# Optimization experiments

Measured on AMD Instinct MI355X. Metric: run time of the kernel, lower is better.

## Reference

```python
import jax, jax.numpy as jnp
import numpy as np


def _seg_mean(feat_src, src, dst, n_tgt):
    # gather neighbor features along edges, scatter-mean onto targets
    g = feat_src[src]                                   # [E, D]
    s = jax.ops.segment_sum(g, dst, num_segments=n_tgt)  # [n_tgt, D]
    cnt = jax.ops.segment_sum(jnp.ones((src.shape[0],), feat_src.dtype), dst,
                              num_segments=n_tgt)
    return s / jnp.clip(cnt, 1.0)[:, None]


def setup_inputs() -> dict:
    key = jax.random.key(0)
    ks = jax.random.split(key, 12)
    N0, N1, N2 = 1000000, 400000, 100000
    E0, E1 = 2000000, 500000
    D, H, O = 128, 50, 1
    return {
        "x": jax.random.normal(ks[0], (N0, D), jnp.float32),
        "edge_attr": jnp.ones((N0,), jnp.float32),  # unused by forward, kept for signature parity
        "src0": jax.random.randint(ks[1], (E0,), 0, N0),
        "dst0": jax.random.randint(ks[2], (E0,), 0, N1),
        "src1": jax.random.randint(ks[3], (E1,), 0, N1),
        "dst1": jax.random.randint(ks[4], (E1,), 0, N2),
        "n1": N1,
        "n2": N2,
        "Wl1": jax.random.normal(ks[5], (D, H), jnp.float32) / np.sqrt(D),
        "bl1": jnp.zeros((H,), jnp.float32),
        "Wr1": jax.random.normal(ks[6], (D, H), jnp.float32) / np.sqrt(D),
        "Wl2": jax.random.normal(ks[7], (H, H), jnp.float32) / np.sqrt(H),
        "bl2": jnp.zeros((H,), jnp.float32),
        "Wr2": jax.random.normal(ks[8], (H, H), jnp.float32) / np.sqrt(H),
        "Wo": jax.random.normal(ks[9], (H, O), jnp.float32) / np.sqrt(H),
        "bo": jnp.zeros((O,), jnp.float32),
    }


def reference(x, edge_attr, src0, dst0, src1, dst1, n1, n2,
              Wl1, bl1, Wr1, Wl2, bl2, Wr2, Wo, bo):
    # Layer 1: SAGEConv((x, x[:n1]), edge_index0)  -> [n1, H]
    agg1 = _seg_mean(x, src0, dst0, n1)
    h = agg1 @ Wl1 + bl1 + x[:n1] @ Wr1
    h = jax.nn.relu(h)  # inter-layer ReLU (dropout p=0.0 is a no-op)
    # Layer 2: SAGEConv((h, h[:n2]), edge_index1)  -> [n2, H]
    agg2 = _seg_mean(h, src1, dst1, n2)
    h2 = agg2 @ Wl2 + bl2 + h[:n2] @ Wr2
    # Final Linear + ReLU
    return jax.nn.relu(h2 @ Wo + bo)
```

## Files before the change

### kernel.cpp

```cpp
#include <hip/hip_runtime.h>

#define N0V 1000000
#define N1V 400000
#define N2V 100000
#define E0V 2000000
#define E1V 500000
#define DD  128
#define HH  50
#define FP  64
#define KC  32
#define NB_SCAN 1563

#define OFF_DEG    0ULL
#define OFF_SSUM   1600000ULL
#define OFF_CNT2   2000000ULL
#define ZERO_BYTES 2400000ULL
#define OFF_ROWPTR 2400000ULL
#define OFF_CURSOR 4000000ULL
#define OFF_BSUM   5600000ULL
#define OFF_SMALL  5608192ULL
#define OFF_WL1P   5609216ULL
#define OFF_WR1P   5641984ULL
#define OFF_S      5674752ULL
#define OFF_T      7274752ULL
#define OFF_CSR    7674752ULL
#define OFF_AGG    15674752ULL
#define OFF_Y      118074752ULL
#define WS_NEEDED  246074752ULL

__device__ inline unsigned short f2bf(float f) {
    unsigned int u = __float_as_uint(f);
    unsigned int r = (u + 0x7FFFu + ((u >> 16) & 1u)) >> 16;
    return (unsigned short)r;
}

__global__ void pad_w(const float* __restrict__ Wl1, const float* __restrict__ Wr1,
                      const float* __restrict__ bl1,
                      const float* __restrict__ Wl2, const float* __restrict__ bl2,
                      const float* __restrict__ Wr2, const float* __restrict__ Wo,
                      const float* __restrict__ bo,
                      float* __restrict__ Wl1p, float* __restrict__ Wr1p,
                      float* __restrict__ smalls)
{
    int gid = blockIdx.x * 256 + threadIdx.x;
    if (gid < 128 * FP) {
        int k = gid >> 6, f = gid & 63;
        float a = (f < HH) ? Wl1[k * HH + f] : 0.f;
        float b = (f < HH) ? Wr1[k * HH + f] : 0.f;
        Wl1p[gid] = a;
        Wr1p[gid] = b;
    }
    if (gid < FP) {
        float a = 0.f, b = 0.f;
        if (gid < HH) {
            for (int g = 0; g < HH; ++g) {
                float w = Wo[g];
                a += Wl2[gid * HH + g] * w;
                b += Wr2[gid * HH + g] * w;
            }
        }
        smalls[gid]          = (gid < HH) ? bl1[gid] : 0.f;
        smalls[FP + gid]     = a;
        smalls[2 * FP + gid] = b;
    }
    if (gid == 0) {
        float c = bo[0];
        for (int g = 0; g < HH; ++g) c += bl2[g] * Wo[g];
        smalls[3 * FP] = c;
    }
}

__global__ __launch_bounds__(256, 4) void gemm_y(const float* __restrict__ X,
                                                 const float* __restrict__ Wp,
                                                 unsigned int* __restrict__ Ybf)
{
    __shared__ float xs[KC * 256];
    const int t  = threadIdx.x;
    const int n0 = blockIdx.x * 256;
    const int ng = t >> 3;
    const int fg = t & 7;
    const int nbase = n0 + ng * 8;

    float acc[8][8];
#pragma unroll
    for (int i = 0; i < 8; ++i)
#pragma unroll
        for (int j = 0; j < 8; ++j) acc[i][j] = 0.f;

    for (int c = 0; c < DD / KC; ++c) {
        if (c) __syncthreads();
#pragma unroll
        for (int j = 0; j < 8; ++j) {
            int f4  = j * 256 + t;
            int row = f4 >> 3;
            int c4  = f4 & 7;
            int gn  = n0 + row;
            float4 v = make_float4(0.f, 0.f, 0.f, 0.f);
            if (gn < N0V) v = *(const float4*)(X + (size_t)gn * DD + c * KC + c4 * 4);
            int kb  = c4 * 4;
            int rsw = row ^ (c4 << 3);
            xs[(kb + 0) * 256 + rsw] = v.x;
            xs[(kb + 1) * 256 + rsw] = v.y;
            xs[(kb + 2) * 256 + rsw] = v.z;
            xs[(kb + 3) * 256 + rsw] = v.w;
        }
        __syncthreads();
#pragma unroll 4
        for (int kk = 0; kk < KC; ++kk) {
            int m = kk >> 2;
            const float* xp = &xs[kk * 256 + ((ng ^ m) << 3)];
            float4 x0 = *(const float4*)xp;
            float4 x1 = *(const float4*)(xp + 4);
            const float* wr = Wp + (size_t)(c * KC + kk) * FP + fg * 8;
            float4 w0 = *(const float4*)wr;
            float4 w1 = *(const float4*)(wr + 4);
            float xv[8] = {x0.x, x0.y, x0.z, x0.w, x1.x, x1.y, x1.z, x1.w};
            float wv[8] = {w0.x, w0.y, w0.z, w0.w, w1.x, w1.y, w1.z, w1.w};
#pragma unroll
            for (int i = 0; i < 8; ++i)
#pragma unroll
                for (int j = 0; j < 8; ++j)
                    acc[i][j] = fmaf(xv[i], wv[j], acc[i][j]);
        }
    }

    if (nbase < N0V) {
#pragma unroll
        for (int i = 0; i < 8; ++i) {
            uint4 q;
            q.x = (unsigned)f2bf(acc[i][0]) | ((unsigned)f2bf(acc[i][1]) << 16);
            q.y = (unsigned)f2bf(acc[i][2]) | ((unsigned)f2bf(acc[i][3]) << 16);
            q.z = (unsigned)f2bf(acc[i][4]) | ((unsigned)f2bf(acc[i][5]) << 16);
            q.w = (unsigned)f2bf(acc[i][6]) | ((unsigned)f2bf(acc[i][7]) << 16);
            *(uint4*)(Ybf + (size_t)(nbase + i) * 32 + fg * 4) = q;
        }
    }
}

__global__ __launch_bounds__(256) void hist1(const int* __restrict__ dst,
                                             int* __restrict__ deg)
{
    int e = blockIdx.x * 256 + threadIdx.x;
    if (e < E0V) atomicAdd(&deg[dst[e]], 1);
}

__global__ __launch_bounds__(256) void scan_a(const int* __restrict__ deg,
                                              int* __restrict__ incl,
                                              int* __restrict__ bsum)
{
    __shared__ int s[256];
    int tid = threadIdx.x;
    int i = blockIdx.x * 256 + tid;
    int v = (i < N1V) ? deg[i] : 0;
    s[tid] = v;
    __syncthreads();
#pragma unroll
    for (int off = 1; off < 256; off <<= 1) {
        int tv = (tid >= off) ? s[tid - off] : 0;
        __syncthreads();
        s[tid] += tv;
        __syncthreads();
    }
    if (i < N1V) incl[i] = s[tid];
    if (tid == 255) bsum[blockIdx.x] = s[255];
}

__global__ __launch_bounds__(256) void scan_b(int* __restrict__ bsum)
{
    __shared__ int s[256];
    __shared__ int run_s;
    int tid = threadIdx.x;
    if (tid == 0) run_s = 0;
    __syncthreads();
    for (int base = 0; base < NB_SCAN; base += 256) {
        int idx = base + tid;
        int v = (idx < NB_SCAN) ? bsum[idx] : 0;
        s[tid] = v;
        __syncthreads();
#pragma unroll
        for (int off = 1; off < 256; off <<= 1) {
            int tv = (tid >= off) ? s[tid - off] : 0;
            __syncthreads();
            s[tid] += tv;
            __syncthreads();
        }
        int rbase = run_s;
        if (idx < NB_SCAN) bsum[idx] = s[tid] - v + rbase;
        __syncthreads();
        if (tid == 255) run_s = rbase + s[255];
        __syncthreads();
    }
}

__global__ __launch_bounds__(256) void scan_c(const int* __restrict__ deg,
                                              int* __restrict__ rowptr,
                                              int* __restrict__ cursor,
                                              const int* __restrict__ bsum)
{
    int i = blockIdx.x * 256 + threadIdx.x;
    if (i < N1V) {
        int ex = rowptr[i] - deg[i] + bsum[blockIdx.x];
        rowptr[i] = ex;
        cursor[i] = ex;
    }
}

__global__ __launch_bounds__(256) void fill1(const int* __restrict__ src,
                                             const int* __restrict__ dst,
                                             int* __restrict__ cursor,
                                             int* __restrict__ csr)
{
    int e = blockIdx.x * 256 + threadIdx.x;
    if (e < E0V) {
        int d = dst[e];
        int pos = atomicAdd(&cursor[d], 1);
        csr[pos] = src[e];
    }
}

__global__ __launch_bounds__(256) void gather1(const unsigned int* __restrict__ Ybf,
                                               const int* __restrict__ rowptr,
                                               const int* __restrict__ deg,
                                               const int* __restrict__ csr,
                                               float* __restrict__ agg)
{
    int node = blockIdx.x * 8 + (threadIdx.x >> 5);
    int lane = threadIdx.x & 31;
    if (node >= N1V) return;
    int start = rowptr[node];
    int dg = deg[node];
    float a0 = 0.f, a1 = 0.f, b0 = 0.f, b1 = 0.f;
    int k = 0;
    for (; k + 1 < dg; k += 2) {
        int s0 = csr[start + k];
        int s1 = csr[start + k + 1];
        unsigned v0 = Ybf[(size_t)s0 * 32 + lane];
        unsigned v1 = Ybf[(size_t)s1 * 32 + lane];
        a0 += __uint_as_float(v0 << 16);
        a1 += __uint_as_float(v0 & 0xFFFF0000u);
        b0 += __uint_as_float(v1 << 16);
        b1 += __uint_as_float(v1 & 0xFFFF0000u);
    }
    if (k < dg) {
        int s0 = csr[start + k];
        unsigned v0 = Ybf[(size_t)s0 * 32 + lane];
        a0 += __uint_as_float(v0 << 16);
        a1 += __uint_as_float(v0 & 0xFFFF0000u);
    }
    a0 += b0;
    a1 += b1;
    float inv = 1.0f / (float)max(dg, 1);
    *(float2*)(agg + (size_t)node * FP + lane * 2) = make_float2(a0 * inv, a1 * inv);
}

__global__ __launch_bounds__(256, 4) void node_l1(const float* __restrict__ X,
                                                  const float* __restrict__ Wp,
                                                  const float* __restrict__ agg,
                                                  const float* __restrict__ smalls,
                                                  float* __restrict__ sArr,
                                                  float* __restrict__ tArr)
{
    __shared__ float xs[KC * 256];
    const int t  = threadIdx.x;
    const int n0 = blockIdx.x * 256;
    const int ng = t >> 3;
    const int fg = t & 7;
    const int nbase = n0 + ng * 8;

    float acc[8][8];
#pragma unroll
    for (int i = 0; i < 8; ++i)
#pragma unroll
        for (int j = 0; j < 8; ++j) acc[i][j] = 0.f;

    for (int c = 0; c < DD / KC; ++c) {
        if (c) __syncthreads();
#pragma unroll
        for (int j = 0; j < 8; ++j) {
            int f4  = j * 256 + t;
            int row = f4 >> 3;
            int c4  = f4 & 7;
            int gn  = n0 + row;
            float4 v = make_float4(0.f, 0.f, 0.f, 0.f);
            if (gn < N1V) v = *(const float4*)(X + (size_t)gn * DD + c * KC + c4 * 4);
            int kb  = c4 * 4;
            int rsw = row ^ (c4 << 3);
            xs[(kb + 0) * 256 + rsw] = v.x;
            xs[(kb + 1) * 256 + rsw] = v.y;
            xs[(kb + 2) * 256 + rsw] = v.z;
            xs[(kb + 3) * 256 + rsw] = v.w;
        }
        __syncthreads();
#pragma unroll 4
        for (int kk = 0; kk < KC; ++kk) {
            int m = kk >> 2;
            const float* xp = &xs[kk * 256 + ((ng ^ m) << 3)];
            float4 x0 = *(const float4*)xp;
            float4 x1 = *(const float4*)(xp + 4);
            const float* wr = Wp + (size_t)(c * KC + kk) * FP + fg * 8;
            float4 w0 = *(const float4*)wr;
            float4 w1 = *(const float4*)(wr + 4);
            float xv[8] = {x0.x, x0.y, x0.z, x0.w, x1.x, x1.y, x1.z, x1.w};
            float wv[8] = {w0.x, w0.y, w0.z, w0.w, w1.x, w1.y, w1.z, w1.w};
#pragma unroll
            for (int i = 0; i < 8; ++i)
#pragma unroll
                for (int j = 0; j < 8; ++j)
                    acc[i][j] = fmaf(xv[i], wv[j], acc[i][j]);
        }
    }

    if (nbase >= N1V) return;

    const float* blp = smalls + fg * 8;
    const float* wAp = smalls + FP + fg * 8;
    const float* wBp = smalls + 2 * FP + fg * 8;
    float bl_r[8], wA_r[8], wB_r[8];
#pragma unroll
    for (int j = 0; j < 8; ++j) { bl_r[j] = blp[j]; wA_r[j] = wAp[j]; wB_r[j] = wBp[j]; }

    float ps[8], pt[8];
#pragma unroll
    for (int i = 0; i < 8; ++i) {
        int n = nbase + i;
        const float* ar = agg + (size_t)n * FP + fg * 8;
        float4 a0 = *(const float4*)ar;
        float4 a1 = *(const float4*)(ar + 4);
        float agf[8] = {a0.x, a0.y, a0.z, a0.w, a1.x, a1.y, a1.z, a1.w};
        float s_acc = 0.f, t_acc = 0.f;
#pragma unroll
        for (int j = 0; j < 8; ++j) {
            float h = fmaxf(agf[j] + bl_r[j] + acc[i][j], 0.f);
            s_acc = fmaf(h, wA_r[j], s_acc);
            t_acc = fmaf(h, wB_r[j], t_acc);
        }
        ps[i] = s_acc; pt[i] = t_acc;
    }
#pragma unroll
    for (int i = 0; i < 8; ++i) {
#pragma unroll
        for (int m = 1; m < 8; m <<= 1) {
            ps[i] += __shfl_xor(ps[i], m);
            pt[i] += __shfl_xor(pt[i], m);
        }
    }
    if (fg == 0) {
#pragma unroll
        for (int i = 0; i < 8; ++i) sArr[nbase + i] = ps[i];
        if (nbase < N2V) {
#pragma unroll
            for (int i = 0; i < 8; ++i) tArr[nbase + i] = pt[i];
        }
    }
}

__global__ __launch_bounds__(256) void scatter2(const float* __restrict__ sArr,
                                                const int* __restrict__ src,
                                                const int* __restrict__ dst,
                                                float* __restrict__ ssum,
                                                float* __restrict__ cnt2)
{
    int e = blockIdx.x * 256 + threadIdx.x;
    if (e >= E1V) return;
    int sI = src[e];
    int dI = dst[e];
    atomicAdd(&ssum[dI], sArr[sI]);
    atomicAdd(&cnt2[dI], 1.0f);
}

__global__ __launch_bounds__(256) void final_out(const float* __restrict__ ssum,
                                                 const float* __restrict__ cnt2,
                                                 const float* __restrict__ tArr,
                                                 const float* __restrict__ smalls,
                                                 float* __restrict__ out)
{
    int i = blockIdx.x * 256 + threadIdx.x;
    if (i >= N2V) return;
    float c = smalls[3 * FP];
    float inv = 1.0f / fmaxf(cnt2[i], 1.0f);
    float o = fmaf(ssum[i], inv, tArr[i] + c);
    out[i] = fmaxf(o, 0.f);
}

extern "C" void kernel_launch(void* const* d_in, const int* in_sizes, int n_in,
                              void* d_out, int out_size, void* d_ws, size_t ws_size,
                              hipStream_t stream)
{
    if (ws_size < WS_NEEDED) return;

    const float* x    = (const float*)d_in[0];
    const int*   src0 = (const int*)d_in[2];
    const int*   dst0 = (const int*)d_in[3];
    const int*   src1 = (const int*)d_in[4];
    const int*   dst1 = (const int*)d_in[5];
    const float* Wl1  = (const float*)d_in[8];
    const float* bl1  = (const float*)d_in[9];
    const float* Wr1  = (const float*)d_in[10];
    const float* Wl2  = (const float*)d_in[11];
    const float* bl2  = (const float*)d_in[12];
    const float* Wr2  = (const float*)d_in[13];
    const float* Wo   = (const float*)d_in[14];
    const float* bo   = (const float*)d_in[15];
    float* out = (float*)d_out;

    char* ws = (char*)d_ws;
    int*   deg    = (int*)(ws + OFF_DEG);
    float* ssum   = (float*)(ws + OFF_SSUM);
    float* cnt2   = (float*)(ws + OFF_CNT2);
    int*   rowptr = (int*)(ws + OFF_ROWPTR);
    int*   cursor = (int*)(ws + OFF_CURSOR);
    int*   bsum   = (int*)(ws + OFF_BSUM);
    float* smalls = (float*)(ws + OFF_SMALL);
    float* Wl1p   = (float*)(ws + OFF_WL1P);
    float* Wr1p   = (float*)(ws + OFF_WR1P);
    float* sArr   = (float*)(ws + OFF_S);
    float* tArr   = (float*)(ws + OFF_T);
    int*   csr    = (int*)(ws + OFF_CSR);
    float* agg    = (float*)(ws + OFF_AGG);
    unsigned int* ybf = (unsigned int*)(ws + OFF_Y);

    hipMemsetAsync(d_ws, 0, ZERO_BYTES, stream);

    pad_w<<<32, 256, 0, stream>>>(Wl1, Wr1, bl1, Wl2, bl2, Wr2, Wo, bo, Wl1p, Wr1p, smalls);

    gemm_y<<<(N0V + 255) / 256, 256, 0, stream>>>(x, Wl1p, ybf);

    hist1<<<(E0V + 255) / 256, 256, 0, stream>>>(dst0, deg);
    scan_a<<<NB_SCAN, 256, 0, stream>>>(deg, rowptr, bsum);
    scan_b<<<1, 256, 0, stream>>>(bsum);
    scan_c<<<NB_SCAN, 256, 0, stream>>>(deg, rowptr, cursor, bsum);
    fill1<<<(E0V + 255) / 256, 256, 0, stream>>>(src0, dst0, cursor, csr);

    gather1<<<(N1V + 7) / 8, 256, 0, stream>>>(ybf, rowptr, deg, csr, agg);

    node_l1<<<NB_SCAN, 256, 0, stream>>>(x, Wr1p, agg, smalls, sArr, tArr);

    scatter2<<<(E1V + 255) / 256, 256, 0, stream>>>(sArr, src1, dst1, ssum, cnt2);

    final_out<<<(N2V + 255) / 256, 256, 0, stream>>>(ssum, cnt2, tArr, smalls, out);
}
```

Baseline: 1.490 ms.

## Fuse both layer-1 GEMMs into one MFMA fp16 kernel with fp16 intermediates

Replaces the two scalar FP32 GEMM kernels (x@Wl1 for all nodes and x[:n1]@Wr1) with one kernel that converts x tiles to fp16 in shared memory and uses 16x16x32 f16 MFMA instructions. It computes both products in a single pass over x, removing the second read of x[:n1]. Y, the root term D and the aggregated features are now stored as packed fp16 rather than bf16/fp32, and a lightweight epilogue kernel replaces node_l1. This targets the FLOP-bound scalar GEMM and redundant x reads, at the cost of reduced precision and a larger D buffer.

New measurement: 1.237 ms. 1.21x faster.

```diff
diff --git a/kernel.cpp b/kernel.cpp
--- a/kernel.cpp
+++ b/kernel.cpp
@@ -8,7 +8,6 @@
 #define DD  128
 #define HH  50
 #define FP  64
-#define KC  32
 #define NB_SCAN 1563
 
 #define OFF_DEG    0ULL
@@ -19,19 +18,30 @@
 #define OFF_CURSOR 4000000ULL
 #define OFF_BSUM   5600000ULL
 #define OFF_SMALL  5608192ULL
-#define OFF_WL1P   5609216ULL
-#define OFF_WR1P   5641984ULL
-#define OFF_S      5674752ULL
-#define OFF_T      7274752ULL
-#define OFF_CSR    7674752ULL
-#define OFF_AGG    15674752ULL
-#define OFF_Y      118074752ULL
-#define WS_NEEDED  246074752ULL
-
-__device__ inline unsigned short f2bf(float f) {
-    unsigned int u = __float_as_uint(f);
-    unsigned int r = (u + 0x7FFFu + ((u >> 16) & 1u)) >> 16;
-    return (unsigned short)r;
+#define OFF_WLT    5609216ULL
+#define OFF_WRT    5625600ULL
+#define OFF_S      5641984ULL
+#define OFF_T      7241984ULL
+#define OFF_CSR    7641984ULL
+#define OFF_AGG    15641984ULL
+#define OFF_D      66841984ULL
+#define OFF_Y      118041984ULL
+#define WS_NEEDED  246041984ULL
+
+typedef _Float16 half8 __attribute__((ext_vector_type(8)));
+typedef _Float16 half4 __attribute__((ext_vector_type(4)));
+typedef float    f32x4 __attribute__((ext_vector_type(4)));
+
+__device__ inline unsigned pack2h(float a, float b) {
+    union { _Float16 h[2]; unsigned u; } cv;
+    cv.h[0] = (_Float16)a;
+    cv.h[1] = (_Float16)b;
+    return cv.u;
+}
+__device__ inline float2 unp2h(unsigned v) {
+    union { unsigned u; _Float16 h[2]; } cv;
+    cv.u = v;
+    return make_float2((float)cv.h[0], (float)cv.h[1]);
 }
 
 __global__ void pad_w(const float* __restrict__ Wl1, const float* __restrict__ Wr1,
@@ -39,16 +49,16 @@
                       const float* __restrict__ Wl2, const float* __restrict__ bl2,
                       const float* __restrict__ Wr2, const float* __restrict__ Wo,
                       const float* __restrict__ bo,
-                      float* __restrict__ Wl1p, float* __restrict__ Wr1p,
+                      _Float16* __restrict__ Wlt, _Float16* __restrict__ Wrt,
                       float* __restrict__ smalls)
 {
     int gid = blockIdx.x * 256 + threadIdx.x;
-    if (gid < 128 * FP) {
-        int k = gid >> 6, f = gid & 63;
-        float a = (f < HH) ? Wl1[k * HH + f] : 0.f;
-        float b = (f < HH) ? Wr1[k * HH + f] : 0.f;
-        Wl1p[gid] = a;
-        Wr1p[gid] = b;
+    if (gid < 64 * 128) {
+        int n = gid >> 7, k = gid & 127;
+        float a = (n < HH) ? Wl1[k * HH + n] : 0.f;
+        float b = (n < HH) ? Wr1[k * HH + n] : 0.f;
+        Wlt[gid] = (_Float16)a;
+        Wrt[gid] = (_Float16)b;
     }
     if (gid < FP) {
         float a = 0.f, b = 0.f;
@@ -70,69 +80,97 @@
     }
 }
 
-__global__ __launch_bounds__(256, 4) void gemm_y(const float* __restrict__ X,
-                                                 const float* __restrict__ Wp,
-                                                 unsigned int* __restrict__ Ybf)
-{
-    __shared__ float xs[KC * 256];
+__global__ __launch_bounds__(256, 3) void fused_gemm(
+    const float* __restrict__ X,
+    const _Float16* __restrict__ Wlt,
+    const _Float16* __restrict__ Wrt,
+    unsigned int* __restrict__ Yh,
+    unsigned int* __restrict__ Dh)
+{
+    __shared__ _Float16 xs[128][72];
     const int t  = threadIdx.x;
-    const int n0 = blockIdx.x * 256;
-    const int ng = t >> 3;
-    const int fg = t & 7;
-    const int nbase = n0 + ng * 8;
-
-    float acc[8][8];
-#pragma unroll
-    for (int i = 0; i < 8; ++i)
-#pragma unroll
-        for (int j = 0; j < 8; ++j) acc[i][j] = 0.f;
-
-    for (int c = 0; c < DD / KC; ++c) {
+    const int w  = t >> 6;
+    const int l  = t & 63;
+    const int lr = l & 15;
+    const int lk = l >> 4;
+    const int n0 = blockIdx.x * 128;
+    const bool hasD = (blockIdx.x < N1V / 128);
+
+    f32x4 yacc[4][2], dacc[4][2];
+#pragma unroll
+    for (int ft = 0; ft < 4; ++ft)
+#pragma unroll
+        for (int mt = 0; mt < 2; ++mt) {
+            yacc[ft][mt] = (f32x4){0.f, 0.f, 0.f, 0.f};
+            dacc[ft][mt] = (f32x4){0.f, 0.f, 0.f, 0.f};
+        }
+
+    const int srow = t >> 4;
+    const int scol = t & 15;
+
+    for (int c = 0; c < 2; ++c) {
         if (c) __syncthreads();
 #pragma unroll
-        for (int j = 0; j < 8; ++j) {
-            int f4  = j * 256 + t;
-            int row = f4 >> 3;
-            int c4  = f4 & 7;
+        for (int p = 0; p < 8; ++p) {
+            int row = p * 16 + srow;
             int gn  = n0 + row;
             float4 v = make_float4(0.f, 0.f, 0.f, 0.f);
-            if (gn < N0V) v = *(const float4*)(X + (size_t)gn * DD + c * KC + c4 * 4);
-            int kb  = c4 * 4;
-            int rsw = row ^ (c4 << 3);
-            xs[(kb + 0) * 256 + rsw] = v.x;
-            xs[(kb + 1) * 256 + rsw] = v.y;
-            xs[(kb + 2) * 256 + rsw] = v.z;
-            xs[(kb + 3) * 256 + rsw] = v.w;
-        }
-        __syncthreads();
-#pragma unroll 4
-        for (int kk = 0; kk < KC; ++kk) {
-            int m = kk >> 2;
-            const float* xp = &xs[kk * 256 + ((ng ^ m) << 3)];
-            float4 x0 = *(const float4*)xp;
-            float4 x1 = *(const float4*)(xp + 4);
-            const float* wr = Wp + (size_t)(c * KC + kk) * FP + fg * 8;
-            float4 w0 = *(const float4*)wr;
-            float4 w1 = *(const float4*)(wr + 4);
-            float xv[8] = {x0.x, x0.y, x0.z, x0.w, x1.x, x1.y, x1.z, x1.w};
-            float wv[8] = {w0.x, w0.y, w0.z, w0.w, w1.x, w1.y, w1.z, w1.w};
-#pragma unroll
-            for (int i = 0; i < 8; ++i)
-#pragma unroll
-                for (int j = 0; j < 8; ++j)
-                    acc[i][j] = fmaf(xv[i], wv[j], acc[i][j]);
-        }
-    }
-
-    if (nbase < N0V) {
-#pragma unroll
-        for (int i = 0; i < 8; ++i) {
-            uint4 q;
-            q.x = (unsigned)f2bf(acc[i][0]) | ((unsigned)f2bf(acc[i][1]) << 16);
-            q.y = (unsigned)f2bf(acc[i][2]) | ((unsigned)f2bf(acc[i][3]) << 16);
-            q.z = (unsigned)f2bf(acc[i][4]) | ((unsigned)f2bf(acc[i][5]) << 16);
-            q.w = (unsigned)f2bf(acc[i][6]) | ((unsigned)f2bf(acc[i][7]) << 16);
-            *(uint4*)(Ybf + (size_t)(nbase + i) * 32 + fg * 4) = q;
+            if (gn < N0V) v = *(const float4*)(X + (size_t)gn * DD + c * 64 + scol * 4);
+            half4 h = { (_Float16)v.x, (_Float16)v.y, (_Float16)v.z, (_Float16)v.w };
+            *(half4*)(&xs[row][scol * 4]) = h;
+        }
+        __syncthreads();
+#pragma unroll
+        for (int ks = 0; ks < 2; ++ks) {
+            half8 xf[2];
+#pragma unroll
+            for (int mt = 0; mt < 2; ++mt)
+                xf[mt] = *(const half8*)(&xs[w * 32 + mt * 16 + lr][ks * 32 + lk * 8]);
+            const int kg = c * 64 + ks * 32 + lk * 8;
+#pragma unroll
+            for (int ft = 0; ft < 4; ++ft) {
+                half8 wl = *(const half8*)(Wlt + (ft * 16 + lr) * 128 + kg);
+#pragma unroll
+                for (int mt = 0; mt < 2; ++mt)
+                    yacc[ft][mt] = __builtin_amdgcn_mfma_f32_16x16x32_f16(
+                        wl, xf[mt], yacc[ft][mt], 0, 0, 0);
+            }
+            if (hasD) {
+#pragma unroll
+                for (int ft = 0; ft < 4; ++ft) {
+                    half8 wr = *(const half8*)(Wrt + (ft * 16 + lr) * 128 + kg);
+#pragma unroll
+                    for (int mt = 0; mt < 2; ++mt)
+                        dacc[ft][mt] = __builtin_amdgcn_mfma_f32_16x16x32_f16(
+                            wr, xf[mt], dacc[ft][mt], 0, 0, 0);
+                }
+            }
+        }
+    }
+
+#pragma unroll
+    for (int mt = 0; mt < 2; ++mt) {
+        int node = n0 + w * 32 + mt * 16 + lr;
+        if (node >= N0V) continue;
+        unsigned int* yp = Yh + (size_t)node * 32 + lk * 2;
+#pragma unroll
+        for (int ft = 0; ft < 4; ++ft) {
+            f32x4 a = yacc[ft][mt];
+            uint2 q;
+            q.x = pack2h(a[0], a[1]);
+            q.y = pack2h(a[2], a[3]);
+            *(uint2*)(yp + ft * 8) = q;
+        }
+        if (hasD) {
+            unsigned int* dp = Dh + (size_t)node * 32 + lk * 2;
+#pragma unroll
+            for (int ft = 0; ft < 4; ++ft) {
+                f32x4 a = dacc[ft][mt];
+                uint2 q;
+                q.x = pack2h(a[0], a[1]);
+                q.y = pack2h(a[2], a[3]);
+                *(uint2*)(dp + ft * 8) = q;
+            }
         }
     }
 }
@@ -218,11 +256,11 @@
     }
 }
 
-__global__ __launch_bounds__(256) void gather1(const unsigned int* __restrict__ Ybf,
+__global__ __launch_bounds__(256) void gather1(const unsigned int* __restrict__ Yh,
                                                const int* __restrict__ rowptr,
                                                const int* __restrict__ deg,
                                                const int* __restrict__ csr,
-                                               float* __restrict__ agg)
+                                               unsigned int* __restrict__ aggh)
 {
     int node = blockIdx.x * 8 + (threadIdx.x >> 5);
     int lane = threadIdx.x & 31;
@@ -234,123 +272,68 @@
     for (; k + 1 < dg; k += 2) {
         int s0 = csr[start + k];
         int s1 = csr[start + k + 1];
-        unsigned v0 = Ybf[(size_t)s0 * 32 + lane];
-        unsigned v1 = Ybf[(size_t)s1 * 32 + lane];
-        a0 += __uint_as_float(v0 << 16);
-        a1 += __uint_as_float(v0 & 0xFFFF0000u);
-        b0 += __uint_as_float(v1 << 16);
-        b1 += __uint_as_float(v1 & 0xFFFF0000u);
+        unsigned v0 = Yh[(size_t)s0 * 32 + lane];
+        unsigned v1 = Yh[(size_t)s1 * 32 + lane];
+        float2 f0 = unp2h(v0);
+        float2 f1 = unp2h(v1);
+        a0 += f0.x; a1 += f0.y;
+        b0 += f1.x; b1 += f1.y;
     }
     if (k < dg) {
         int s0 = csr[start + k];
-        unsigned v0 = Ybf[(size_t)s0 * 32 + lane];
-        a0 += __uint_as_float(v0 << 16);
-        a1 += __uint_as_float(v0 & 0xFFFF0000u);
+        float2 f0 = unp2h(Yh[(size_t)s0 * 32 + lane]);
+        a0 += f0.x; a1 += f0.y;
     }
     a0 += b0;
     a1 += b1;
     float inv = 1.0f / (float)max(dg, 1);
-    *(float2*)(agg + (size_t)node * FP + lane * 2) = make_float2(a0 * inv, a1 * inv);
-}
-
-__global__ __launch_bounds__(256, 4) void node_l1(const float* __restrict__ X,
-                                                  const float* __restrict__ Wp,
-                                                  const float* __restrict__ agg,
-                                                  const float* __restrict__ smalls,
-                                                  float* __restrict__ sArr,
-                                                  float* __restrict__ tArr)
-{
-    __shared__ float xs[KC * 256];
-    const int t  = threadIdx.x;
-    const int n0 = blockIdx.x * 256;
-    const int ng = t >> 3;
-    const int fg = t & 7;
-    const int nbase = n0 + ng * 8;
-
-    float acc[8][8];
-#pragma unroll
-    for (int i = 0; i < 8; ++i)
-#pragma unroll
-        for (int j = 0; j < 8; ++j) acc[i][j] = 0.f;
-
-    for (int c = 0; c < DD / KC; ++c) {
-        if (c) __syncthreads();
-#pragma unroll
-        for (int j = 0; j < 8; ++j) {
-            int f4  = j * 256 + t;
-            int row = f4 >> 3;
-            int c4  = f4 & 7;
-            int gn  = n0 + row;
-            float4 v = make_float4(0.f, 0.f, 0.f, 0.f);
-            if (gn < N1V) v = *(const float4*)(X + (size_t)gn * DD + c * KC + c4 * 4);
-            int kb  = c4 * 4;
-            int rsw = row ^ (c4 << 3);
-            xs[(kb + 0) * 256 + rsw] = v.x;
-            xs[(kb + 1) * 256 + rsw] = v.y;
-            xs[(kb + 2) * 256 + rsw] = v.z;
-            xs[(kb + 3) * 256 + rsw] = v.w;
-        }
-        __syncthreads();
-#pragma unroll 4
-        for (int kk = 0; kk < KC; ++kk) {
-            int m = kk >> 2;
-            const float* xp = &xs[kk * 256 + ((ng ^ m) << 3)];
-            float4 x0 = *(const float4*)xp;
-            float4 x1 = *(const float4*)(xp + 4);
-            const float* wr = Wp + (size_t)(c * KC + kk) * FP + fg * 8;
-            float4 w0 = *(const float4*)wr;
-            float4 w1 = *(const float4*)(wr + 4);
-            float xv[8] = {x0.x, x0.y, x0.z, x0.w, x1.x, x1.y, x1.z, x1.w};
-            float wv[8] = {w0.x, w0.y, w0.z, w0.w, w1.x, w1.y, w1.z, w1.w};
-#pragma unroll
-            for (int i = 0; i < 8; ++i)
-#pragma unroll
-                for (int j = 0; j < 8; ++j)
-                    acc[i][j] = fmaf(xv[i], wv[j], acc[i][j]);
-        }
-    }
-
-    if (nbase >= N1V) return;
+    aggh[(size_t)node * 32 + lane] = pack2h(a0 * inv, a1 * inv);
+}
+
+__global__ __launch_bounds__(256) void epilogue2(const unsigned int* __restrict__ aggh,
+                                                 const unsigned int* __restrict__ Dh,
+                                                 const float* __restrict__ smalls,
+                                                 float* __restrict__ sArr,
+                                                 float* __restrict__ tArr)
+{
+    int t  = threadIdx.x;
+    int ng = t >> 3;
+    int fg = t & 7;
+    int node = blockIdx.x * 32 + ng;
+    if (node >= N1V) return;
+
+    uint4 av = *(const uint4*)(aggh + (size_t)node * 32 + fg * 4);
+    uint4 dv = *(const uint4*)(Dh   + (size_t)node * 32 + fg * 4);
 
     const float* blp = smalls + fg * 8;
     const float* wAp = smalls + FP + fg * 8;
     const float* wBp = smalls + 2 * FP + fg * 8;
-    float bl_r[8], wA_r[8], wB_r[8];
-#pragma unroll
-    for (int j = 0; j < 8; ++j) { bl_r[j] = blp[j]; wA_r[j] = wAp[j]; wB_r[j] = wBp[j]; }
-
-    float ps[8], pt[8];
-#pragma unroll
-    for (int i = 0; i < 8; ++i) {
-        int n = nbase + i;
-        const float* ar = agg + (size_t)n * FP + fg * 8;
-        float4 a0 = *(const float4*)ar;
-        float4 a1 = *(const float4*)(ar + 4);
-        float agf[8] = {a0.x, a0.y, a0.z, a0.w, a1.x, a1.y, a1.z, a1.w};
-        float s_acc = 0.f, t_acc = 0.f;
-#pragma unroll
-        for (int j = 0; j < 8; ++j) {
-            float h = fmaxf(agf[j] + bl_r[j] + acc[i][j], 0.f);
-            s_acc = fmaf(h, wA_r[j], s_acc);
-            t_acc = fmaf(h, wB_r[j], t_acc);
-        }
-        ps[i] = s_acc; pt[i] = t_acc;
-    }
-#pragma unroll
-    for (int i = 0; i < 8; ++i) {
-#pragma unroll
-        for (int m = 1; m < 8; m <<= 1) {
-            ps[i] += __shfl_xor(ps[i], m);
-            pt[i] += __shfl_xor(pt[i], m);
-        }
+
+    float af[8], df[8];
+    { float2 f; f = unp2h(av.x); af[0]=f.x; af[1]=f.y;
+      f = unp2h(av.y); af[2]=f.x; af[3]=f.y;
+      f = unp2h(av.z); af[4]=f.x; af[5]=f.y;
+      f = unp2h(av.w); af[6]=f.x; af[7]=f.y;
+      f = unp2h(dv.x); df[0]=f.x; df[1]=f.y;
+      f = unp2h(dv.y); df[2]=f.x; df[3]=f.y;
+      f = unp2h(dv.z); df[4]=f.x; df[5]=f.y;
+      f = unp2h(dv.w); df[6]=f.x; df[7]=f.y; }
+
+    float s_acc = 0.f, t_acc = 0.f;
+#pragma unroll
+    for (int j = 0; j < 8; ++j) {
+        float h = fmaxf(af[j] + blp[j] + df[j], 0.f);
+        s_acc = fmaf(h, wAp[j], s_acc);
+        t_acc = fmaf(h, wBp[j], t_acc);
+    }
+#pragma unroll
+    for (int m = 1; m < 8; m <<= 1) {
+        s_acc += __shfl_xor(s_acc, m);
+        t_acc += __shfl_xor(t_acc, m);
     }
     if (fg == 0) {
-#pragma unroll
-        for (int i = 0; i < 8; ++i) sArr[nbase + i] = ps[i];
-        if (nbase < N2V) {
-#pragma unroll
-            for (int i = 0; i < 8; ++i) tArr[nbase + i] = pt[i];
-        }
+        sArr[node] = s_acc;
+        if (node < N2V) tArr[node] = t_acc;
     }
 }
 
@@ -411,19 +394,20 @@
     int*   cursor = (int*)(ws + OFF_CURSOR);
     int*   bsum   = (int*)(ws + OFF_BSUM);
     float* smalls = (float*)(ws + OFF_SMALL);
-    float* Wl1p   = (float*)(ws + OFF_WL1P);
-    float* Wr1p   = (float*)(ws + OFF_WR1P);
+    _Float16* Wlt = (_Float16*)(ws + OFF_WLT);
+    _Float16* Wrt = (_Float16*)(ws + OFF_WRT);
     float* sArr   = (float*)(ws + OFF_S);
     float* tArr   = (float*)(ws + OFF_T);
     int*   csr    = (int*)(ws + OFF_CSR);
-    float* agg    = (float*)(ws + OFF_AGG);
-    unsigned int* ybf = (unsigned int*)(ws + OFF_Y);
+    unsigned int* aggh = (unsigned int*)(ws + OFF_AGG);
+    unsigned int* Dh   = (unsigned int*)(ws + OFF_D);
+    unsigned int* Yh   = (unsigned int*)(ws + OFF_Y);
 
     hipMemsetAsync(d_ws, 0, ZERO_BYTES, stream);
 
-    pad_w<<<32, 256, 0, stream>>>(Wl1, Wr1, bl1, Wl2, bl2, Wr2, Wo, bo, Wl1p, Wr1p, smalls);
-
-    gemm_y<<<(N0V + 255) / 256, 256, 0, stream>>>(x, Wl1p, ybf);
+    pad_w<<<32, 256, 0, stream>>>(Wl1, Wr1, bl1, Wl2, bl2, Wr2, Wo, bo, Wlt, Wrt, smalls);
+
+    fused_gemm<<<(N0V + 127) / 128, 256, 0, stream>>>(x, Wlt, Wrt, Yh, Dh);
 
     hist1<<<(E0V + 255) / 256, 256, 0, stream>>>(dst0, deg);
     scan_a<<<NB_SCAN, 256, 0, stream>>>(deg, rowptr, bsum);
@@ -431,9 +415,9 @@
     scan_c<<<NB_SCAN, 256, 0, stream>>>(deg, rowptr, cursor, bsum);
     fill1<<<(E0V + 255) / 256, 256, 0, stream>>>(src0, dst0, cursor, csr);
 
-    gather1<<<(N1V + 7) / 8, 256, 0, stream>>>(ybf, rowptr, deg, csr, agg);
-
-    node_l1<<<NB_SCAN, 256, 0, stream>>>(x, Wr1p, agg, smalls, sArr, tArr);
+    gather1<<<(N1V + 7) / 8, 256, 0, stream>>>(Yh, rowptr, deg, csr, aggh);
+
+    epilogue2<<<(N1V + 31) / 32, 256, 0, stream>>>(aggh, Dh, smalls, sArr, tArr);
 
     scatter2<<<(E1V + 255) / 256, 256, 0, stream>>>(sArr, src1, dst1, ssum, cnt2);
 
```
